# Optimization experiments

Measured on AMD Instinct MI355X. Metric: run time of the kernel, lower is better.

Reference implementation:

```python
import jax, jax.numpy as jnp
import numpy as np

H, DH = 8, 16  # num_heads, head_dim (out_feats // num_heads)
NP, NA, NS = 100000, 60000, 1000


def _gat_conv(feat_src, feat_dst, n_dst, src, dst, W, al, ar, b):
    # DGL GATConv (eval mode: feat_drop/attn_drop are identity)
    hs = (feat_src @ W).reshape(-1, H, DH)          # [Ns,H,D]
    hd = (feat_dst @ W).reshape(-1, H, DH)          # [Nd,H,D]
    el = (hs * al).sum(-1)                          # [Ns,H]
    er = (hd * ar).sum(-1)                          # [Nd,H]
    e = jax.nn.leaky_relu(el[src] + er[dst], negative_slope=0.2)  # [E,H]
    # segment softmax over edges sharing a destination node
    emax = jax.ops.segment_max(e, dst, num_segments=n_dst)
    emax = jnp.where(jnp.isfinite(emax), emax, 0.0)
    ee = jnp.exp(e - emax[dst])
    denom = jax.ops.segment_sum(ee, dst, num_segments=n_dst)
    alpha = ee / jnp.maximum(denom[dst], 1e-9)      # [E,H]
    m = jax.ops.segment_sum(alpha[:, :, None] * hs[src], dst, num_segments=n_dst)
    return m.reshape(n_dst, H * DH) + b             # [Nd, out_feats]


def setup_inputs() -> dict:
    key = jax.random.key(0)
    ks = jax.random.split(key, 18)
    Epa, Eps = 300000, 150000
    f32 = jnp.float32
    inp = {
        "feat_paper_0": jax.random.normal(ks[0], (NP, 128), f32),
        "feat_author_0": jax.random.normal(ks[1], (NA, 128), f32),
        "feat_subject_0": jax.random.normal(ks[2], (NS, 128), f32),
        "feat_paper_1": jax.random.normal(ks[3], (NP, 128), f32),
        "feat_author_1": jax.random.normal(ks[4], (NA, 128), f32),
        "feat_subject_1": jax.random.normal(ks[5], (NS, 128), f32),
        "pa_src": jax.random.randint(ks[6], (Epa,), 0, NP, jnp.int32),
        "pa_dst": jax.random.randint(ks[7], (Epa,), 0, NA, jnp.int32),
        "ap_src": jax.random.randint(ks[8], (Epa,), 0, NA, jnp.int32),
        "ap_dst": jax.random.randint(ks[9], (Epa,), 0, NP, jnp.int32),
        "ps_src": jax.random.randint(ks[10], (Eps,), 0, NP, jnp.int32),
        "ps_dst": jax.random.randint(ks[11], (Eps,), 0, NS, jnp.int32),
        "sp_src": jax.random.randint(ks[12], (Eps,), 0, NS, jnp.int32),
        "sp_dst": jax.random.randint(ks[13], (Eps,), 0, NP, jnp.int32),
        "Ws": jax.random.normal(ks[14], (4, 128, 128), f32) * 0.08,
        "als": jax.random.normal(ks[15], (4, H, DH), f32) * 0.1,
        "ars": jax.random.normal(ks[16], (4, H, DH), f32) * 0.1,
        "bs": jnp.zeros((4, 128), f32),
    }
    return inp


def reference(feat_paper_0, feat_author_0, feat_subject_0,
              feat_paper_1, feat_author_1, feat_subject_1,
              pa_src, pa_dst, ap_src, ap_dst, ps_src, ps_dst, sp_src, sp_dst,
              Ws, als, ars, bs):
    def one_input(fp, fa, fs):
        # rel 0: paper->author, 1: author->paper, 2: paper->subject, 3: subject->paper
        h_author = _gat_conv(fp, fa, NA, pa_src, pa_dst, Ws[0], als[0], ars[0], bs[0])
        h_paper_ap = _gat_conv(fa, fp, NP, ap_src, ap_dst, Ws[1], als[1], ars[1], bs[1])
        h_subject = _gat_conv(fp, fs, NS, ps_src, ps_dst, Ws[2], als[2], ars[2], bs[2])
        h_paper_sp = _gat_conv(fs, fp, NP, sp_src, sp_dst, Ws[3], als[3], ars[3], bs[3])
        h_paper = (h_paper_ap + h_paper_sp) * 0.5  # HeteroGraphConv aggregate='mean'
        # act = identity; key order for ACM: [paper, author, subject]
        return jnp.concatenate([h_paper, h_author, h_subject], axis=0)

    out0 = one_input(feat_paper_0, feat_author_0, feat_subject_0)
    out1 = one_input(feat_paper_1, feat_author_1, feat_subject_1)
    return jnp.stack([out0, out1], axis=0)  # [2, NP+NA+NS, 128]
```

## Files before the change

kernel.cpp:

```cpp
#include <hip/hip_runtime.h>

#define NHEAD 8
#define NPAPER 100000
#define NAUTHOR 60000
#define NSUBJ 1000
#define NTOT (NPAPER + NAUTHOR + NSUBJ)
#define NDEG 261000

typedef __attribute__((ext_vector_type(8))) short bf16x8;
typedef __attribute__((ext_vector_type(4))) float f32x4;

__device__ __forceinline__ unsigned short f2bf(float x) {
    unsigned int u = __builtin_bit_cast(unsigned int, x);
    u += 0x7fffu + ((u >> 16) & 1u);
    return (unsigned short)(u >> 16);
}
__device__ __forceinline__ float bf2f_lo(unsigned int v) {
    return __builtin_bit_cast(float, v << 16);
}
__device__ __forceinline__ float bf2f_hi(unsigned int v) {
    return __builtin_bit_cast(float, v & 0xffff0000u);
}

__global__ void prep_kernel(const float* __restrict__ Ws, const float* __restrict__ als,
                            const float* __restrict__ ars,
                            unsigned short* __restrict__ Wt,
                            unsigned short* __restrict__ combo, int* __restrict__ deg) {
    int b = blockIdx.x;
    if (b >= 288) {
        int idx = (b - 288) * 1024 + threadIdx.x * 4;
        if (idx < NDEG) *reinterpret_cast<int4*>(&deg[idx]) = int4{0, 0, 0, 0};
        return;
    }
    int idx = b * 256 + threadIdx.x;
    if (idx < 65536) {
        int r = idx >> 14, rem = idx & 16383, c = rem >> 7, k = rem & 127;
        Wt[idx] = f2bf(Ws[(r << 14) + k * 128 + c]);
    } else if (idx < 65536 + 8192) {
        int j = idx - 65536;
        int r = j >> 11, rem = j & 2047, n = rem >> 7, k = rem & 127;
        int p = r ^ 1;
        const float *W, *a;
        if (n < 8) {
            W = Ws + (r << 14) + k * 128 + n * 16;
            a = als + r * 128 + n * 16;
        } else {
            int h = n - 8;
            W = Ws + (p << 14) + k * 128 + h * 16;
            a = ars + p * 128 + h * 16;
        }
        float s = 0.f;
#pragma unroll
        for (int d = 0; d < 16; ++d) s += W[d] * a[d];
        combo[j] = f2bf(s);
    }
}

struct EdgePtrs {
    const int* esrc[4];
    const int* edst[4];
    int ebase[5];
    int nbase[4];
};

__global__ void csr_count(EdgePtrs cp, int* __restrict__ deg) {
    int idx = blockIdx.x * 256 + threadIdx.x;
    if (idx >= cp.ebase[4]) return;
    int r = 0;
    while (idx >= cp.ebase[r + 1]) ++r;
    atomicAdd(&deg[cp.nbase[r] + cp.edst[r][idx - cp.ebase[r]]], 1);
}

__global__ __launch_bounds__(256) void scan_bsum(const int* __restrict__ deg,
                                                 int* __restrict__ bsums, int N) {
    int base = blockIdx.x * 1024 + threadIdx.x * 4;
    int s = 0;
#pragma unroll
    for (int j = 0; j < 4; ++j) {
        int i = base + j;
        if (i < N) s += deg[i];
    }
#pragma unroll
    for (int off = 32; off; off >>= 1) s += __shfl_down(s, off);
    __shared__ int wt[4];
    if ((threadIdx.x & 63) == 0) wt[threadIdx.x >> 6] = s;
    __syncthreads();
    if (threadIdx.x == 0) bsums[blockIdx.x] = wt[0] + wt[1] + wt[2] + wt[3];
}

__global__ __launch_bounds__(256) void scan_final(const int* __restrict__ deg,
                                                  const int* __restrict__ bsums,
                                                  int* __restrict__ row_ptr,
                                                  int* __restrict__ cursor, int N) {
    int t = threadIdx.x;
    __shared__ int s_start;
    __shared__ int wsum[4];
    {
        int acc = 0;
        for (int i = t; i < (int)blockIdx.x; i += 256) acc += bsums[i];
#pragma unroll
        for (int off = 32; off; off >>= 1) acc += __shfl_down(acc, off);
        if ((t & 63) == 0) wsum[t >> 6] = acc;
        __syncthreads();
        if (t == 0) s_start = wsum[0] + wsum[1] + wsum[2] + wsum[3];
        __syncthreads();
    }
    int base = blockIdx.x * 1024 + t * 4;
    int d[4];
    int s = 0;
#pragma unroll
    for (int j = 0; j < 4; ++j) {
        int i = base + j;
        d[j] = (i < N) ? deg[i] : 0;
        s += d[j];
    }
    int inc = s;
#pragma unroll
    for (int off = 1; off < 64; off <<= 1) {
        int u = __shfl_up(inc, off);
        if ((t & 63) >= off) inc += u;
    }
    __shared__ int wt[4];
    if ((t & 63) == 63) wt[t >> 6] = inc;
    __syncthreads();
    int start = s_start;
    for (int w = 0; w < (t >> 6); ++w) start += wt[w];
    start += inc - s;
#pragma unroll
    for (int j = 0; j < 4; ++j) {
        int i = base + j;
        if (i < N) {
            row_ptr[i] = start;
            cursor[i] = start;
        }
        start += d[j];
    }
    if (base < N && base + 4 >= N) row_ptr[N] = start;
}

__device__ __forceinline__ void stage_W512(unsigned short* Wl,
                                           const unsigned short* __restrict__ Wt,
                                           const unsigned short* __restrict__ cb,
                                           int tid) {
#pragma unroll
    for (int it = 0; it < 5; ++it) {
        int id = it * 512 + tid;
        if (id < 2304) {
            int r = id >> 4, c8 = id & 15;
            const unsigned short* srcp =
                (r < 128) ? (Wt + r * 128) : (cb + (r - 128) * 128);
            uint4 v = *reinterpret_cast<const uint4*>(srcp + c8 * 8);
            *reinterpret_cast<uint4*>(&Wl[(r * 16 + (c8 ^ (r & 15))) * 8]) = v;
        }
    }
}

__device__ __forceinline__ void mfma_set512(const unsigned short* Wl,
                                            unsigned short* Abf, const bf16x8* af,
                                            int tid, int row0, int N,
                                            float* __restrict__ el,
                                            float* __restrict__ er) {
    const int l = tid & 63, w = tid >> 6, lrow = l & 15, lk8 = l >> 4;
#pragma unroll
    for (int t9 = 0; t9 < 9; ++t9) {
        f32x4 acc = f32x4{0.f, 0.f, 0.f, 0.f};
#pragma unroll
        for (int ks = 0; ks < 4; ++ks) {
            int wrow = t9 * 16 + lrow;
            int c8 = ks * 4 + lk8;
            bf16x8 bf = *reinterpret_cast<const bf16x8*>(
                &Wl[(wrow * 16 + (c8 ^ (wrow & 15))) * 8]);
            acc = __builtin_amdgcn_mfma_f32_16x16x32_bf16(af[ks], bf, acc, 0, 0, 0);
        }
        if (t9 < 8) {
#pragma unroll
            for (int r = 0; r < 4; ++r) {
                int rl = w * 16 + lk8 * 4 + r;
                int col = t9 * 16 + lrow;
                Abf[(rl * 16 + ((col >> 3) ^ (rl & 15))) * 8 + (col & 7)] = f2bf(acc[r]);
            }
        } else {
#pragma unroll
            for (int r = 0; r < 4; ++r) {
                int row = row0 + w * 16 + lk8 * 4 + r;
                if (row < N) {
                    if (lrow < 8) el[(size_t)row * 8 + lrow] = acc[r];
                    else er[(size_t)row * 8 + (lrow - 8)] = acc[r];
                }
            }
        }
    }
}

__device__ __forceinline__ void store_hs512(const unsigned short* Abf,
                                            unsigned short* __restrict__ hs, int tid,
                                            int row0, int N) {
#pragma unroll
    for (int it = 0; it < 4; ++it) {
        int id = it * 512 + tid;
        int r = id >> 4, c8 = id & 15;
        int row = row0 + r;
        if (row < N) {
            uint4 v = *reinterpret_cast<const uint4*>(&Abf[(r * 16 + (c8 ^ (r & 15))) * 8]);
            *reinterpret_cast<uint4*>(hs + (size_t)row * 128 + c8 * 8) = v;
        }
    }
}

struct SPArgs {
    const int* esrc[4];
    const int* edst[4];
    int ebase[5];
    int nbase[4];
    int* cursor;
    int* scsr;
    int sblk;
    const float* A[6];
    int N[6];
    int blk0[7];
    const unsigned short* Wt1[6];
    const unsigned short* cb1[6];
    unsigned short* hs1[6];
    float* el1[6];
    float* er1[6];
    const unsigned short* Wt2[6];
    const unsigned short* cb2[6];
    unsigned short* hs2[6];
    float* el2[6];
    float* er2[6];
    int has2[6];
};

__global__ __launch_bounds__(512) void scatter_project(SPArgs a) {
    __shared__ unsigned short Abf[128 * 128];
    __shared__ unsigned short Wl[144 * 128];
    int bb = blockIdx.x;
    const int tid = threadIdx.x;
    if (bb < a.sblk) {
        int idx = bb * 512 + tid;
        if (idx < a.ebase[4]) {
            int r = 0;
            while (idx >= a.ebase[r + 1]) ++r;
            int e = idx - a.ebase[r];
            int p = atomicAdd(&a.cursor[a.nbase[r] + a.edst[r][e]], 1);
            a.scsr[p] = a.esrc[r][e];
        }
        return;
    }
    bb -= a.sblk;
    int t = 0;
    while (bb >= a.blk0[t + 1]) ++t;
    const int row0 = (bb - a.blk0[t]) * 128;
    const int N = a.N[t];
    const float* A = a.A[t];

#pragma unroll
    for (int it = 0; it < 4; ++it) {
        int id = it * 512 + tid;
        int r = id >> 4, c8 = id & 15;
        int row = row0 + r;
        if (row >= N) row = N - 1;
        const f32x4* ap = reinterpret_cast<const f32x4*>(A + (size_t)row * 128 + c8 * 8);
        f32x4 v0 = __builtin_nontemporal_load(ap);
        f32x4 v1 = __builtin_nontemporal_load(ap + 1);
        uint4 pk;
        pk.x = (unsigned)f2bf(v0.x) | ((unsigned)f2bf(v0.y) << 16);
        pk.y = (unsigned)f2bf(v0.z) | ((unsigned)f2bf(v0.w) << 16);
        pk.z = (unsigned)f2bf(v1.x) | ((unsigned)f2bf(v1.y) << 16);
        pk.w = (unsigned)f2bf(v1.z) | ((unsigned)f2bf(v1.w) << 16);
        *reinterpret_cast<uint4*>(&Abf[(r * 16 + (c8 ^ (r & 15))) * 8]) = pk;
    }
    stage_W512(Wl, a.Wt1[t], a.cb1[t], tid);
    __syncthreads();

    const int l = tid & 63, w = tid >> 6, lrow = l & 15, lk8 = l >> 4;
    bf16x8 af[4];
    const int arow = w * 16 + lrow;
#pragma unroll
    for (int ks = 0; ks < 4; ++ks) {
        int c8 = ks * 4 + lk8;
        af[ks] = *reinterpret_cast<const bf16x8*>(
            &Abf[(arow * 16 + (c8 ^ (arow & 15))) * 8]);
    }
    __syncthreads();

    mfma_set512(Wl, Abf, af, tid, row0, N, a.el1[t], a.er1[t]);
    __syncthreads();
    store_hs512(Abf, a.hs1[t], tid, row0, N);
    if (!a.has2[t]) return;
    stage_W512(Wl, a.Wt2[t], a.cb2[t], tid);
    __syncthreads();
    mfma_set512(Wl, Abf, af, tid, row0, N, a.el2[t], a.er2[t]);
    __syncthreads();
    store_hs512(Abf, a.hs2[t], tid, row0, N);
}

__device__ __forceinline__ void acc_dual(
    int p0, int p1, float erd0, float erd1, int l, int h,
    const int* __restrict__ srcs,
    const float* __restrict__ el0, const float* __restrict__ el1,
    const unsigned short* __restrict__ hs0, const unsigned short* __restrict__ hs1,
    float* A0, float* A1, float& DS0, float& DS1) {
    float a0[8], a1[8];
#pragma unroll
    for (int j = 0; j < 8; ++j) { a0[j] = 0.f; a1[j] = 0.f; }
    float d0 = 0.f, d1 = 0.f;
    int p = p0;
    for (; p + 4 <= p1; p += 4) {
        int sx[4];
#pragma unroll
        for (int u = 0; u < 4; ++u) sx[u] = srcs[p + u];
        float ev0[4], ev1[4];
        uint4 q0[4], q1[4];
#pragma unroll
        for (int u = 0; u < 4; ++u) {
            ev0[u] = el0[(size_t)sx[u] * 8 + h] + erd0;
            ev1[u] = el1[(size_t)sx[u] * 8 + h] + erd1;
            q0[u] = *reinterpret_cast<const uint4*>(hs0 + (size_t)sx[u] * 128 + l * 8);
            q1[u] = *reinterpret_cast<const uint4*>(hs1 + (size_t)sx[u] * 128 + l * 8);
        }
#pragma unroll
        for (int u = 0; u < 4; ++u) {
            float e0 = ev0[u];
            e0 = e0 > 0.f ? e0 : 0.2f * e0;
            float ee0 = __expf(e0);
            d0 += ee0;
            a0[0] += ee0 * bf2f_lo(q0[u].x);
            a0[1] += ee0 * bf2f_hi(q0[u].x);
            a0[2] += ee0 * bf2f_lo(q0[u].y);
            a0[3] += ee0 * bf2f_hi(q0[u].y);
            a0[4] += ee0 * bf2f_lo(q0[u].z);
            a0[5] += ee0 * bf2f_hi(q0[u].z);
            a0[6] += ee0 * bf2f_lo(q0[u].w);
            a0[7] += ee0 * bf2f_hi(q0[u].w);
            float e1 = ev1[u];
            e1 = e1 > 0.f ? e1 : 0.2f * e1;
            float ee1 = __expf(e1);
            d1 += ee1;
            a1[0] += ee1 * bf2f_lo(q1[u].x);
            a1[1] += ee1 * bf2f_hi(q1[u].x);
            a1[2] += ee1 * bf2f_lo(q1[u].y);
            a1[3] += ee1 * bf2f_hi(q1[u].y);
            a1[4] += ee1 * bf2f_lo(q1[u].z);
            a1[5] += ee1 * bf2f_hi(q1[u].z);
            a1[6] += ee1 * bf2f_lo(q1[u].w);
            a1[7] += ee1 * bf2f_hi(q1[u].w);
        }
    }
    for (; p < p1; ++p) {
        int s = srcs[p];
        float e0 = el0[(size_t)s * 8 + h] + erd0;
        float e1 = el1[(size_t)s * 8 + h] + erd1;
        uint4 q0 = *reinterpret_cast<const uint4*>(hs0 + (size_t)s * 128 + l * 8);
        uint4 q1 = *reinterpret_cast<const uint4*>(hs1 + (size_t)s * 128 + l * 8);
        e0 = e0 > 0.f ? e0 : 0.2f * e0;
        float ee0 = __expf(e0);
        d0 += ee0;
        a0[0] += ee0 * bf2f_lo(q0.x);
        a0[1] += ee0 * bf2f_hi(q0.x);
        a0[2] += ee0 * bf2f_lo(q0.y);
        a0[3] += ee0 * bf2f_hi(q0.y);
        a0[4] += ee0 * bf2f_lo(q0.z);
        a0[5] += ee0 * bf2f_hi(q0.z);
        a0[6] += ee0 * bf2f_lo(q0.w);
        a0[7] += ee0 * bf2f_hi(q0.w);
        e1 = e1 > 0.f ? e1 : 0.2f * e1;
        float ee1 = __expf(e1);
        d1 += ee1;
        a1[0] += ee1 * bf2f_lo(q1.x);
        a1[1] += ee1 * bf2f_hi(q1.x);
        a1[2] += ee1 * bf2f_lo(q1.y);
        a1[3] += ee1 * bf2f_hi(q1.y);
        a1[4] += ee1 * bf2f_lo(q1.z);
        a1[5] += ee1 * bf2f_hi(q1.z);
        a1[6] += ee1 * bf2f_lo(q1.w);
        a1[7] += ee1 * bf2f_hi(q1.w);
    }
#pragma unroll
    for (int j = 0; j < 8; ++j) { A0[j] = a0[j]; A1[j] = a1[j]; }
    DS0 = d0;
    DS1 = d1;
}

__device__ __forceinline__ void nt_store2(float* op, f32x4 o0, f32x4 o1) {
    f32x4* vp = reinterpret_cast<f32x4*>(op);
    __builtin_nontemporal_store(o0, vp);
    __builtin_nontemporal_store(o1, vp + 1);
}

#define PB2 6250
#define AB2 3750
#define SB2 1000

struct AggArgs {
    const int* rp;
    const int* srcs;
    const float* el[8];
    const float* er[8];
    const unsigned short* hs[8];
    const float* bs;
    float* out0;
    float* out1;
};

__global__ __launch_bounds__(256) void mega_agg(AggArgs a) {
    int blk = blockIdx.x;
    __shared__ float Am[16][128];
    __shared__ float Dm[16][8];

    if (blk < PB2) {
        int dst = blk * 16 + (threadIdx.x >> 4);
        int l = threadIdx.x & 15, h = l >> 1;
        if (dst >= NPAPER) return;
        float A1_0[8], A1_1[8], d1_0, d1_1;
        acc_dual(a.rp[60000 + dst], a.rp[60000 + dst + 1],
                 a.er[1][(size_t)dst * 8 + h], a.er[5][(size_t)dst * 8 + h], l, h,
                 a.srcs, a.el[1], a.el[5], a.hs[1], a.hs[5], A1_0, A1_1, d1_0, d1_1);
        float A3_0[8], A3_1[8], d3_0, d3_1;
        acc_dual(a.rp[161000 + dst], a.rp[161000 + dst + 1],
                 a.er[3][(size_t)dst * 8 + h], a.er[7][(size_t)dst * 8 + h], l, h,
                 a.srcs, a.el[3], a.el[7], a.hs[3], a.hs[7], A3_0, A3_1, d3_0, d3_1);
        const float4* bp1 = reinterpret_cast<const float4*>(a.bs + 128 + l * 8);
        const float4* bp3 = reinterpret_cast<const float4*>(a.bs + 384 + l * 8);
        float4 b10 = bp1[0], b11 = bp1[1], b30 = bp3[0], b31 = bp3[1];
        float i1 = 1.f / fmaxf(d1_0, 1e-9f);
        float i3 = 1.f / fmaxf(d3_0, 1e-9f);
        f32x4 o0, o1;
        o0.x = 0.5f * ((A1_0[0] * i1 + b10.x) + (A3_0[0] * i3 + b30.x));
        o0.y = 0.5f * ((A1_0[1] * i1 + b10.y) + (A3_0[1] * i3 + b30.y));
        o0.z = 0.5f * ((A1_0[2] * i1 + b10.z) + (A3_0[2] * i3 + b30.z));
        o0.w = 0.5f * ((A1_0[3] * i1 + b10.w) + (A3_0[3] * i3 + b30.w));
        o1.x = 0.5f * ((A1_0[4] * i1 + b11.x) + (A3_0[4] * i3 + b31.x));
        o1.y = 0.5f * ((A1_0[5] * i1 + b11.y) + (A3_0[5] * i3 + b31.y));
        o1.z = 0.5f * ((A1_0[6] * i1 + b11.z) + (A3_0[6] * i3 + b31.z));
        o1.w = 0.5f * ((A1_0[7] * i1 + b11.w) + (A3_0[7] * i3 + b31.w));
        nt_store2(a.out0 + (size_t)dst * 128 + l * 8, o0, o1);
        i1 = 1.f / fmaxf(d1_1, 1e-9f);
        i3 = 1.f / fmaxf(d3_1, 1e-9f);
        o0.x = 0.5f * ((A1_1[0] * i1 + b10.x) + (A3_1[0] * i3 + b30.x));
        o0.y = 0.5f * ((A1_1[1] * i1 + b10.y) + (A3_1[1] * i3 + b30.y));
        o0.z = 0.5f * ((A1_1[2] * i1 + b10.z) + (A3_1[2] * i3 + b30.z));
        o0.w = 0.5f * ((A1_1[3] * i1 + b10.w) + (A3_1[3] * i3 + b30.w));
        o1.x = 0.5f * ((A1_1[4] * i1 + b11.x) + (A3_1[4] * i3 + b31.x));
        o1.y = 0.5f * ((A1_1[5] * i1 + b11.y) + (A3_1[5] * i3 + b31.y));
        o1.z = 0.5f * ((A1_1[6] * i1 + b11.z) + (A3_1[6] * i3 + b31.z));
        o1.w = 0.5f * ((A1_1[7] * i1 + b11.w) + (A3_1[7] * i3 + b31.w));
        nt_store2(a.out1 + (size_t)dst * 128 + l * 8, o0, o1);
    } else if (blk < PB2 + AB2) {
        int dst = (blk - PB2) * 16 + (threadIdx.x >> 4);
        int l = threadIdx.x & 15, h = l >> 1;
        if (dst >= NAUTHOR) return;
        float A0[8], A1[8], d0, d1;
        acc_dual(a.rp[dst], a.rp[dst + 1],
                 a.er[0][(size_t)dst * 8 + h], a.er[4][(size_t)dst * 8 + h], l, h,
                 a.srcs, a.el[0], a.el[4], a.hs[0], a.hs[4], A0, A1, d0, d1);
        const float4* bp = reinterpret_cast<const float4*>(a.bs + l * 8);
        float4 b0 = bp[0], b1 = bp[1];
        float inv = 1.f / fmaxf(d0, 1e-9f);
        f32x4 o0 = {A0[0] * inv + b0.x, A0[1] * inv + b0.y,
                    A0[2] * inv + b0.z, A0[3] * inv + b0.w};
        f32x4 o1 = {A0[4] * inv + b1.x, A0[5] * inv + b1.y,
                    A0[6] * inv + b1.z, A0[7] * inv + b1.w};
        nt_store2(a.out0 + (size_t)(NPAPER + dst) * 128 + l * 8, o0, o1);
        inv = 1.f / fmaxf(d1, 1e-9f);
        o0 = f32x4{A1[0] * inv + b0.x, A1[1] * inv + b0.y,
                   A1[2] * inv + b0.z, A1[3] * inv + b0.w};
        o1 = f32x4{A1[4] * inv + b1.x, A1[5] * inv + b1.y,
                   A1[6] * inv + b1.z, A1[7] * inv + b1.w};
        nt_store2(a.out1 + (size_t)(NPAPER + dst) * 128 + l * 8, o0, o1);
    } else {
        int dst = blk - (PB2 + AB2);
        int gl = threadIdx.x >> 4;
        int inp = gl >> 3, ck = gl & 7;
        int l = threadIdx.x & 15, h = l >> 1;
        const float* el = a.el[inp * 4 + 2];
        const float* er = a.er[inp * 4 + 2];
        const unsigned short* hs = a.hs[inp * 4 + 2];
        int p0 = a.rp[160000 + dst], p1 = a.rp[160000 + dst + 1];
        float erd = er[(size_t)dst * 8 + h];
        float acc8[8];
#pragma unroll
        for (int j = 0; j < 8; ++j) acc8[j] = 0.f;
        float dsum = 0.f;
        for (int p = p0 + ck; p < p1; p += 8) {
            int s = a.srcs[p];
            float e = el[(size_t)s * 8 + h] + erd;
            e = e > 0.f ? e : 0.2f * e;
            float ee = __expf(e);
            uint4 q = *reinterpret_cast<const uint4*>(hs + (size_t)s * 128 + l * 8);
            dsum += ee;
            acc8[0] += ee * bf2f_lo(q.x);
            acc8[1] += ee * bf2f_hi(q.x);
            acc8[2] += ee * bf2f_lo(q.y);
            acc8[3] += ee * bf2f_hi(q.y);
            acc8[4] += ee * bf2f_lo(q.z);
            acc8[5] += ee * bf2f_hi(q.z);
            acc8[6] += ee * bf2f_lo(q.w);
            acc8[7] += ee * bf2f_hi(q.w);
        }
#pragma unroll
        for (int j = 0; j < 8; ++j) Am[gl][l * 8 + j] = acc8[j];
        if ((l & 1) == 0) Dm[gl][h] = dsum;
        __syncthreads();
        int c = threadIdx.x;
        int ci = c >> 7;
        int col = c & 127;
        float s = 0.f, dn = 0.f;
        int hh = col >> 4;
#pragma unroll
        for (int g = 0; g < 8; ++g) {
            s += Am[ci * 8 + g][col];
            dn += Dm[ci * 8 + g][hh];
        }
        float v = s / fmaxf(dn, 1e-9f) + a.bs[256 + col];
        float* outp = (ci ? a.out1 : a.out0) + (size_t)(NPAPER + NAUTHOR + dst) * 128 + col;
        __builtin_nontemporal_store(v, outp);
    }
}

extern "C" void kernel_launch(void* const* d_in, const int* in_sizes, int n_in,
                              void* d_out, int out_size, void* d_ws, size_t ws_size,
                              hipStream_t stream) {
    const float* Ws4 = (const float*)d_in[14];
    const float* als = (const float*)d_in[15];
    const float* ars = (const float*)d_in[16];
    const float* bs = (const float*)d_in[17];
    float* out = (float*)d_out;

    const int Es[4] = {in_sizes[6], in_sizes[8], in_sizes[10], in_sizes[12]};
    const int Nsrcs[4] = {NPAPER, NAUTHOR, NPAPER, NSUBJ};
    const int Ndsts[4] = {NAUTHOR, NPAPER, NSUBJ, NPAPER};
    const int Etot = Es[0] + Es[1] + Es[2] + Es[3];

    char* wsp = (char*)d_ws;
    auto carve = [&](size_t bytes) {
        char* p = wsp;
        wsp += (bytes + 255) & ~(size_t)255;
        return p;
    };
    unsigned short* Wt = (unsigned short*)carve(4 * 16384 * 2);
    unsigned short* combo = (unsigned short*)carve(4 * 2048 * 2);
    unsigned short* hsb[2][4];
    float* elb[2][4];
    float* erb[2][4];
    for (int i = 0; i < 2; ++i)
        for (int r = 0; r < 4; ++r) {
            hsb[i][r] = (unsigned short*)carve((size_t)Nsrcs[r] * 128 * 2);
            elb[i][r] = (float*)carve((size_t)Nsrcs[r] * 8 * 4);
            erb[i][r] = (float*)carve((size_t)Ndsts[r] * 8 * 4);
        }
    int* deg = (int*)carve((size_t)NDEG * 4);
    int* cursor = (int*)carve((size_t)NDEG * 4);
    int* bsums = (int*)carve(1024);
    int* rp = (int*)carve((size_t)(NDEG + 1) * 4);
    int* scsr = (int*)carve((size_t)Etot * 4);

    EdgePtrs ep;
    ep.esrc[0] = (const int*)d_in[6];  ep.edst[0] = (const int*)d_in[7];
    ep.esrc[1] = (const int*)d_in[8];  ep.edst[1] = (const int*)d_in[9];
    ep.esrc[2] = (const int*)d_in[10]; ep.edst[2] = (const int*)d_in[11];
    ep.esrc[3] = (const int*)d_in[12]; ep.edst[3] = (const int*)d_in[13];
    ep.ebase[0] = 0;
    for (int r = 0; r < 4; ++r) ep.ebase[r + 1] = ep.ebase[r] + Es[r];
    ep.nbase[0] = 0;
    ep.nbase[1] = 60000;
    ep.nbase[2] = 160000;
    ep.nbase[3] = 161000;

    prep_kernel<<<288 + (NDEG + 1023) / 1024, 256, 0, stream>>>(Ws4, als, ars, Wt,
                                                                combo, deg);
    csr_count<<<(Etot + 255) / 256, 256, 0, stream>>>(ep, deg);
    int nb = (NDEG + 1023) / 1024;
    scan_bsum<<<nb, 256, 0, stream>>>(deg, bsums, NDEG);
    scan_final<<<nb, 256, 0, stream>>>(deg, bsums, rp, cursor, NDEG);

    SPArgs sp;
    for (int r = 0; r < 4; ++r) {
        sp.esrc[r] = ep.esrc[r];
        sp.edst[r] = ep.edst[r];
        sp.nbase[r] = ep.nbase[r];
    }
    for (int r = 0; r < 5; ++r) sp.ebase[r] = ep.ebase[r];
    sp.cursor = cursor;
    sp.scsr = scsr;
    sp.sblk = (Etot + 511) / 512;

    int blk = 0;
    for (int ti = 0; ti < 6; ++ti) {
        int i = ti & 1;
        int nodeT = ti >> 1;
        const int relOf[3] = {0, 1, 3};
        int r = relOf[nodeT];
        const float* feats[3] = {(const float*)d_in[0 + 3 * i],
                                 (const float*)d_in[1 + 3 * i],
                                 (const float*)d_in[2 + 3 * i]};
        sp.A[ti] = feats[nodeT];
        sp.N[ti] = (nodeT == 0) ? NPAPER : (nodeT == 1 ? NAUTHOR : NSUBJ);
        sp.blk0[ti] = blk;
        blk += (sp.N[ti] + 127) / 128;
        sp.Wt1[ti] = Wt + (size_t)r * 16384;
        sp.cb1[ti] = combo + (size_t)r * 2048;
        sp.hs1[ti] = hsb[i][r];
        sp.el1[ti] = elb[i][r];
        sp.er1[ti] = erb[i][r ^ 1];
        sp.has2[ti] = (nodeT == 0);
        int r2 = 2;
        sp.Wt2[ti] = Wt + (size_t)r2 * 16384;
        sp.cb2[ti] = combo + (size_t)r2 * 2048;
        sp.hs2[ti] = hsb[i][r2];
        sp.el2[ti] = elb[i][r2];
        sp.er2[ti] = erb[i][r2 ^ 1];
    }
    sp.blk0[6] = blk;
    scatter_project<<<sp.sblk + blk, 512, 0, stream>>>(sp);

    AggArgs ag;
    ag.rp = rp;
    ag.srcs = scsr;
    for (int i = 0; i < 2; ++i)
        for (int r = 0; r < 4; ++r) {
            ag.el[i * 4 + r] = elb[i][r];
            ag.er[i * 4 + r] = erb[i][r];
            ag.hs[i * 4 + r] = hsb[i][r];
        }
    ag.bs = bs;
    ag.out0 = out;
    ag.out1 = out + (size_t)NTOT * 128;
    mega_agg<<<PB2 + AB2 + SB2, 256, 0, stream>>>(ag);
}
```

Before: 327.1 us.

## Make projection blocks persistent with register prefetch of next tile

The projection part of scatter_project becomes a persistent grid of up to 512 blocks that loop over 128-row tiles with a stride. Each iteration loads the next tile's fp32 rows into registers while the current tile's MFMA and store work runs, to hide global load latency and cut block launch overhead. The cost is extra register pressure from holding eight float4 values per thread, plus fewer blocks to spread across CUs, which may lower occupancy.

```diff
diff --git a/kernel.cpp b/kernel.cpp
--- a/kernel.cpp
+++ b/kernel.cpp
@@ -215,6 +215,8 @@
     int* cursor;
     int* scsr;
     int sblk;
+    int ntiles;
+    int pstride;
     const float* A[6];
     int N[6];
     int blk0[7];
@@ -234,8 +236,8 @@
 __global__ __launch_bounds__(512) void scatter_project(SPArgs a) {
     __shared__ unsigned short Abf[128 * 128];
     __shared__ unsigned short Wl[144 * 128];
+    const int tid = threadIdx.x;
     int bb = blockIdx.x;
-    const int tid = threadIdx.x;
     if (bb < a.sblk) {
         int idx = bb * 512 + tid;
         if (idx < a.ebase[4]) {
@@ -248,51 +250,74 @@
         return;
     }
     bb -= a.sblk;
-    int t = 0;
-    while (bb >= a.blk0[t + 1]) ++t;
-    const int row0 = (bb - a.blk0[t]) * 128;
-    const int N = a.N[t];
-    const float* A = a.A[t];
-
-#pragma unroll
-    for (int it = 0; it < 4; ++it) {
-        int id = it * 512 + tid;
-        int r = id >> 4, c8 = id & 15;
-        int row = row0 + r;
-        if (row >= N) row = N - 1;
-        const f32x4* ap = reinterpret_cast<const f32x4*>(A + (size_t)row * 128 + c8 * 8);
-        f32x4 v0 = __builtin_nontemporal_load(ap);
-        f32x4 v1 = __builtin_nontemporal_load(ap + 1);
-        uint4 pk;
-        pk.x = (unsigned)f2bf(v0.x) | ((unsigned)f2bf(v0.y) << 16);
-        pk.y = (unsigned)f2bf(v0.z) | ((unsigned)f2bf(v0.w) << 16);
-        pk.z = (unsigned)f2bf(v1.x) | ((unsigned)f2bf(v1.y) << 16);
-        pk.w = (unsigned)f2bf(v1.z) | ((unsigned)f2bf(v1.w) << 16);
-        *reinterpret_cast<uint4*>(&Abf[(r * 16 + (c8 ^ (r & 15))) * 8]) = pk;
-    }
-    stage_W512(Wl, a.Wt1[t], a.cb1[t], tid);
-    __syncthreads();
-
-    const int l = tid & 63, w = tid >> 6, lrow = l & 15, lk8 = l >> 4;
-    bf16x8 af[4];
-    const int arow = w * 16 + lrow;
-#pragma unroll
-    for (int ks = 0; ks < 4; ++ks) {
-        int c8 = ks * 4 + lk8;
-        af[ks] = *reinterpret_cast<const bf16x8*>(
-            &Abf[(arow * 16 + (c8 ^ (arow & 15))) * 8]);
-    }
-    __syncthreads();
-
-    mfma_set512(Wl, Abf, af, tid, row0, N, a.el1[t], a.er1[t]);
-    __syncthreads();
-    store_hs512(Abf, a.hs1[t], tid, row0, N);
-    if (!a.has2[t]) return;
-    stage_W512(Wl, a.Wt2[t], a.cb2[t], tid);
-    __syncthreads();
-    mfma_set512(Wl, Abf, af, tid, row0, N, a.el2[t], a.er2[t]);
-    __syncthreads();
-    store_hs512(Abf, a.hs2[t], tid, row0, N);
+
+    f32x4 pf[8];
+    auto prefetch = [&](int g) {
+        int tt = 0;
+        while (g >= a.blk0[tt + 1]) ++tt;
+        const float* A = a.A[tt];
+        int row0 = (g - a.blk0[tt]) * 128;
+        int N = a.N[tt];
+#pragma unroll
+        for (int it = 0; it < 4; ++it) {
+            int id = it * 512 + tid;
+            int r = id >> 4, c8 = id & 15;
+            int row = row0 + r;
+            if (row >= N) row = N - 1;
+            const f32x4* ap =
+                reinterpret_cast<const f32x4*>(A + (size_t)row * 128 + c8 * 8);
+            pf[2 * it] = __builtin_nontemporal_load(ap);
+            pf[2 * it + 1] = __builtin_nontemporal_load(ap + 1);
+        }
+    };
+
+    if (bb < a.ntiles) prefetch(bb);
+    for (int g = bb; g < a.ntiles; g += a.pstride) {
+        int tt = 0;
+        while (g >= a.blk0[tt + 1]) ++tt;
+        const int row0 = (g - a.blk0[tt]) * 128;
+        const int N = a.N[tt];
+
+        __syncthreads();
+#pragma unroll
+        for (int it = 0; it < 4; ++it) {
+            int id = it * 512 + tid;
+            int r = id >> 4, c8 = id & 15;
+            f32x4 v0 = pf[2 * it], v1 = pf[2 * it + 1];
+            uint4 pk;
+            pk.x = (unsigned)f2bf(v0.x) | ((unsigned)f2bf(v0.y) << 16);
+            pk.y = (unsigned)f2bf(v0.z) | ((unsigned)f2bf(v0.w) << 16);
+            pk.z = (unsigned)f2bf(v1.x) | ((unsigned)f2bf(v1.y) << 16);
+            pk.w = (unsigned)f2bf(v1.z) | ((unsigned)f2bf(v1.w) << 16);
+            *reinterpret_cast<uint4*>(&Abf[(r * 16 + (c8 ^ (r & 15))) * 8]) = pk;
+        }
+        stage_W512(Wl, a.Wt1[tt], a.cb1[tt], tid);
+        __syncthreads();
+
+        const int l = tid & 63, w = tid >> 6, lrow = l & 15, lk8 = l >> 4;
+        bf16x8 af[4];
+        const int arow = w * 16 + lrow;
+#pragma unroll
+        for (int ks = 0; ks < 4; ++ks) {
+            int c8 = ks * 4 + lk8;
+            af[ks] = *reinterpret_cast<const bf16x8*>(
+                &Abf[(arow * 16 + (c8 ^ (arow & 15))) * 8]);
+        }
+        __syncthreads();
+
+        if (g + a.pstride < a.ntiles) prefetch(g + a.pstride);
+
+        mfma_set512(Wl, Abf, af, tid, row0, N, a.el1[tt], a.er1[tt]);
+        __syncthreads();
+        store_hs512(Abf, a.hs1[tt], tid, row0, N);
+        if (a.has2[tt]) {
+            stage_W512(Wl, a.Wt2[tt], a.cb2[tt], tid);
+            __syncthreads();
+            mfma_set512(Wl, Abf, af, tid, row0, N, a.el2[tt], a.er2[tt]);
+            __syncthreads();
+            store_hs512(Abf, a.hs2[tt], tid, row0, N);
+        }
+    }
 }
 
 __device__ __forceinline__ void acc_dual(
@@ -612,7 +637,10 @@
         sp.er2[ti] = erb[i][r2 ^ 1];
     }
     sp.blk0[6] = blk;
-    scatter_project<<<sp.sblk + blk, 512, 0, stream>>>(sp);
+    sp.ntiles = blk;
+    int pblks = blk < 512 ? blk : 512;
+    sp.pstride = pblks;
+    scatter_project<<<sp.sblk + pblks, 512, 0, stream>>>(sp);
 
     AggArgs ag;
     ag.rp = rp;
```

Measured after the change: 330.5 us. No clear change (+1.1%).
